# Performance work log

Measured on AMD Instinct MI355X. Metric: run time of the kernel, lower is better.

## Reference

```python
import jax, jax.numpy as jnp
from jax import lax
import numpy as np

VTH = 0.2
DECAY = 0.25            # LIF membrane decay used by pcdmd slayers.LIFSpike (STBP-style)
DT = 0.001              # norse default integration step
TAU_SYN_INV = 200.0     # norse LSNNParameters defaults
TAU_MEM_INV = 100.0
TAU_ADAPT_INV = 1.0 / 700.0
BETA = 0.0              # module sets beta=0 (no threshold adaptation jumps)
ALPHA = 100.0           # SuperSpike surrogate slope (norse 'super' method)

@jax.custom_vjp
def spike_rect(v):
    # Heaviside forward, rectangular surrogate backward (STBP)
    return (v > 0).astype(v.dtype)

def _sr_fwd(v):
    return spike_rect(v), v

def _sr_bwd(v, g):
    return (g * (jnp.abs(v) < 0.5).astype(g.dtype),)

spike_rect.defvjp(_sr_fwd, _sr_bwd)

@jax.custom_vjp
def spike_super(v):
    # Heaviside forward, SuperSpike surrogate backward (norse 'super')
    return (v > 0).astype(v.dtype)

def _ss_fwd(v):
    return spike_super(v), v

def _ss_bwd(v, g):
    return (g / (ALPHA * jnp.abs(v) + 1.0) ** 2,)

spike_super.defvjp(_ss_fwd, _ss_bwd)

def lif_spike(x):
    # x: [..., T] -> spike train [..., T]
    # u_t = DECAY * u_{t-1} * (1 - o_{t-1}) + x_t ; o_t = H(u_t - VTH)
    xT = jnp.moveaxis(x, -1, 0)  # [T, ...]
    u0 = jnp.zeros(xT.shape[1:], x.dtype)
    def step(carry, xt):
        u, o = carry
        u = DECAY * u * (1.0 - o) + xt
        o = spike_rect(u - VTH)
        return (u, o), o
    _, out = lax.scan(step, (u0, u0), xT)
    return jnp.moveaxis(out, 0, -1)

def lsnn_recurrent(x, w_in, w_rec):
    # x: [T, B, H] input spikes; norse LSNNRecurrent lsnn_step with beta=0, v_th=VTH
    x_in = jnp.einsum('tbh,oh->tbo', x, w_in)  # input current, hoisted out of scan
    B, H = x.shape[1], w_in.shape[0]
    z0 = jnp.zeros((B, H), x.dtype)
    state0 = (z0, z0, z0, jnp.full((B, H), VTH, x.dtype))  # z, v, i, b (b starts at v_th)
    def step(state, xt):
        z, v, i, b = state
        i_jump = i + xt + z @ w_rec.T
        v_dec = v + DT * TAU_MEM_INV * (-v + i_jump)          # v_leak = 0
        i_dec = i_jump - DT * TAU_SYN_INV * i_jump
        b_dec = b + DT * TAU_ADAPT_INV * (VTH - b)
        z_new = spike_super(v_dec - b_dec)
        v_new = (1.0 - z_new) * v_dec                          # v_reset = 0
        b_new = b_dec + z_new * TAU_ADAPT_INV * BETA
        return (z_new, v_new, i_dec, b_new), z_new
    _, out = lax.scan(step, state0, x_in)
    return out  # [T, B, H]

def setup_inputs() -> dict:
    key = jax.random.key(0)
    ks = jax.random.split(key, 7)
    B, T = 64, 8192
    EEG_C, AUD_C, H, OUT = 64, 1, 10, 2
    x = jax.random.normal(ks[0], (B, 1, EEG_C + 2 * AUD_C, T), jnp.float32)
    s_in = 1.0 / float(np.sqrt(EEG_C))
    s_h = 1.0 / float(np.sqrt(H))
    return {
        'x': x,
        'w_front': jax.random.uniform(ks[1], (H, EEG_C), jnp.float32, -s_in, s_in),
        'b_front': jax.random.uniform(ks[2], (H,), jnp.float32, -s_in, s_in),
        'w_in': jax.random.uniform(ks[3], (H, H), jnp.float32, -s_h, s_h),
        'w_rec': jax.random.uniform(ks[4], (H, H), jnp.float32, -s_h, s_h),
        'w_cls': jax.random.uniform(ks[5], (OUT, H), jnp.float32, -s_h, s_h),
        'b_cls': jax.random.uniform(ks[6], (OUT,), jnp.float32, -s_h, s_h),
    }

def reference(x, w_front, b_front, w_in, w_rec, w_cls, b_cls):
    AUD_C = 1
    window_length = x.shape[-1]
    eeg = x[:, 0, AUD_C:-AUD_C, :]                              # [B, 64, T]
    eeg = jnp.einsum('bct,hc->bht', eeg, w_front) + b_front[None, :, None]
    eeg = lif_spike(eeg)                                        # spike_tanh in snn mode
    eeg = jnp.transpose(eeg, (2, 0, 1))                         # [T, B, H]
    z = lsnn_recurrent(eeg, w_in, w_rec)                        # [T, B, H]
    out = jnp.transpose(z, (1, 2, 0))                           # [B, H, T]
    out = jnp.einsum('bht,oh->bot', out, w_cls) + b_cls[None, :, None]
    out = lif_spike(out)                                        # spike_sigmoid in snn mode
    return jnp.sum(out, axis=2) / window_length                 # [B, 2]
```

## Files before the change

### kernel.cpp

```cpp
#include <hip/hip_runtime.h>
#include <cstdint>
#include <cstddef>

#define T_LEN 8192
#define BATCH 64
#define HID   10
#define CH    66
#define EEG   64
#define SM_STRIDE 8384

__global__ void k_front(const float* __restrict__ x, const float* __restrict__ wf_g,
                        const float* __restrict__ bf_g, float* __restrict__ y) {
    __shared__ float wf[EEG][HID];
    __shared__ float bf[HID];
    int tid = threadIdx.x;
    for (int i = tid; i < EEG * HID; i += 256) {
        int h = i / EEG, c = i % EEG;
        wf[c][h] = wf_g[i];
    }
    if (tid < HID) bf[tid] = bf_g[tid];
    __syncthreads();

    int b = blockIdx.y;
    int t4 = (blockIdx.x * 256 + tid) * 4;
    const float* xb = x + ((size_t)b * CH + 1) * T_LEN + t4;
    float acc[4][HID];
#pragma unroll
    for (int j = 0; j < 4; ++j)
#pragma unroll
        for (int h = 0; h < HID; ++h) acc[j][h] = bf[h];
#pragma unroll 4
    for (int c = 0; c < EEG; ++c) {
        float4 xv = *(const float4*)(xb + (size_t)c * T_LEN);
#pragma unroll
        for (int h = 0; h < HID; ++h) {
            float w = wf[c][h];
            acc[0][h] = fmaf(xv.x, w, acc[0][h]);
            acc[1][h] = fmaf(xv.y, w, acc[1][h]);
            acc[2][h] = fmaf(xv.z, w, acc[2][h]);
            acc[3][h] = fmaf(xv.w, w, acc[3][h]);
        }
    }
    float* yo = y + (size_t)b * HID * T_LEN + t4;
#pragma unroll
    for (int h = 0; h < HID; ++h)
        *(float4*)(yo + (size_t)h * T_LEN) =
            make_float4(acc[0][h], acc[1][h], acc[2][h], acc[3][h]);
}

__global__ __launch_bounds__(64) void k_flif(const float* __restrict__ y,
                                             unsigned short* __restrict__ smask) {
    int c    = blockIdx.x >> 4;
    int bq   = blockIdx.x & 15;
    int lane = threadIdx.x;
    int g = lane >> 4, h = lane & 15;
    int b = bq * 4 + g;
    int hh = h < HID ? h : HID - 1;

    if (c == 0) {
        for (int i = lane; i < 4 * 96; i += 64) {
            int j = i / 96, w = i % 96;
            ((unsigned*)(smask + (size_t)(bq * 4 + j) * SM_STRIDE))[w] = 0u;
        }
    }

    int t0 = c * 256;
    int ts = t0 - 32; if (ts < 0) ts = 0;
    int nf = (t0 + 256 - ts) >> 2;
    const float4* yb = (const float4*)(y + ((size_t)b * HID + hh) * T_LEN + ts);

    float4 A = yb[0], B = yb[1];
    float u = 0.f, o = 0.f;
    unsigned short* smb = smask + (size_t)b * SM_STRIDE + 192;
    for (int f = 0; f < nf; ++f) {
        int nx = f + 2; if (nx > nf - 1) nx = nf - 1;
        float4 C = yb[nx];
        float vv[4] = {A.x, A.y, A.z, A.w};
        int tb = ts + f * 4;
#pragma unroll
        for (int k = 0; k < 4; ++k) {
            u = (o > 0.5f) ? vv[k] : fmaf(0.25f, u, vv[k]);
            bool sp = (u > 0.2f);
            o = sp ? 1.0f : 0.0f;
            unsigned long long bal = __ballot(sp);
            int t = tb + k;
            if (t >= t0 && h == 0)
                smb[t] = (unsigned short)((bal >> (g * 16)) & 0x3FFull);
        }
        A = B; B = C;
    }
}

__global__ __launch_bounds__(64) void k_lsnn(
    const unsigned short* __restrict__ smask,
    const float* __restrict__ w_in, const float* __restrict__ w_rec,
    const float* __restrict__ w_cls, const float* __restrict__ b_cls,
    float* __restrict__ out) {
    __shared__ float T[1536];
    int lane = threadIdx.x;
    for (int i = lane; i < 1536; i += 64) {
        int hi = i / 768;
        int rem = i - hi * 768;
        int m = rem / 24, role = rem - m * 24;
        float s = 0.f;
        if (role < 22) {
            const float* wrow = (role < 10) ? (w_in + role * HID)
                              : (role < 12) ? (w_cls + (role - 10) * HID)
                                            : (w_rec + (role - 12) * HID);
#pragma unroll
            for (int j = 0; j < 5; ++j)
                if (m & (1u << j)) s += wrow[hi * 5 + j];
        }
        T[i] = s;
    }
    __syncthreads();

    int q = lane >> 4;
    int r = lane & 15;
    int rr = r < 12 ? r : 11;
    int rrec = 12 + (r < HID ? r : 9);
    int shq = q * 16;
    int id = blockIdx.x * 4 + q;
    int b = id >> 7, chunk = id & 127;

    float bcl = (r == 10 || r == 11) ? b_cls[r - HID] : 0.f;

    const unsigned short* sm = smask + (size_t)b * SM_STRIDE + (size_t)chunk * 64;

    auto xlook = [&](const uint4& mv, float* X) {
        unsigned hw[8] = { mv.x & 0x3FFu, (mv.x >> 16) & 0x3FFu,
                           mv.y & 0x3FFu, (mv.y >> 16) & 0x3FFu,
                           mv.z & 0x3FFu, (mv.z >> 16) & 0x3FFu,
                           mv.w & 0x3FFu, (mv.w >> 16) & 0x3FFu };
#pragma unroll
        for (int u = 0; u < 8; ++u)
            X[u] = T[(hw[u] & 31u) * 24 + rr] + T[768 + (hw[u] >> 5) * 24 + rr];
    };

    uint4 mB = *(const uint4*)(sm + 8);
    uint4 mC = *(const uint4*)(sm + 16);
    uint4 mD = *(const uint4*)(sm + 24);
    float Xc[8], Xn[8], Pc[8], Pn[8];
    { uint4 m0 = *(const uint4*)(sm); xlook(m0, Xc); }
#pragma unroll
    for (int u = 0; u < 8; ++u) { Pc[u] = 0.f; Pn[u] = 0.f; }

    float v = 0.f, cur = 0.f;
    unsigned zmask = 0;
    float uc = 0.f, oc = 0.f, accs = 0.f;

    for (int gr = 0; gr < 32; ++gr) {
        int nb = gr + 4; if (nb > 31) nb = 31;
        uint4 mE = *(const uint4*)(sm + (size_t)nb * 8);
        xlook(mB, Xn);
        unsigned zs[8];
#pragma unroll
        for (int u = 0; u < 8; ++u) {
            float rec = T[(zmask & 31u) * 24 + rrec] + T[768 + (zmask >> 5) * 24 + rrec];
            float ij = (cur + Xc[u]) + rec;
            float vd = v + 0.1f * (ij - v);
            cur = ij - 0.2f * ij;
            bool zb = vd > 0.2f;
            unsigned long long bal = __ballot(zb);
            v = zb ? 0.f : vd;
            zmask = (unsigned)(bal >> shq) & 0x3FFu;
            zs[u] = zmask;
        }
        if (gr >= 21) {
#pragma unroll
            for (int u = 0; u < 8; ++u)
                Pn[u] = T[(zs[u] & 31u) * 24 + rr] + T[768 + (zs[u] >> 5) * 24 + rr];
        }
        if (gr >= 22) {
            bool in = (gr >= 25);
#pragma unroll
            for (int u = 0; u < 8; ++u) {
                float ci = Pc[u] + bcl;
                uc = (oc > 0.5f) ? ci : fmaf(0.25f, uc, ci);
                oc = (uc > 0.2f) ? 1.f : 0.f;
                if (in) accs += oc;
            }
        }
#pragma unroll
        for (int u = 0; u < 8; ++u) { Xc[u] = Xn[u]; Pc[u] = Pn[u]; }
        mB = mC; mC = mD; mD = mE;
    }
#pragma unroll
    for (int u = 0; u < 8; ++u) {
        float ci = Pc[u] + bcl;
        uc = (oc > 0.5f) ? ci : fmaf(0.25f, uc, ci);
        oc = (uc > 0.2f) ? 1.f : 0.f;
        accs += oc;
    }
    if (r == 10 || r == 11)
        atomicAdd(&out[b * 2 + (r - 10)], accs * (1.0f / 8192.0f));
}

extern "C" void kernel_launch(void* const* d_in, const int* in_sizes, int n_in,
                              void* d_out, int out_size, void* d_ws, size_t ws_size,
                              hipStream_t stream) {
    const float* x       = (const float*)d_in[0];
    const float* w_front = (const float*)d_in[1];
    const float* b_front = (const float*)d_in[2];
    const float* w_in    = (const float*)d_in[3];
    const float* w_rec   = (const float*)d_in[4];
    const float* w_cls   = (const float*)d_in[5];
    const float* b_cls   = (const float*)d_in[6];
    float* out = (float*)d_out;

    float* y = (float*)d_ws;
    unsigned short* smask =
        (unsigned short*)((char*)d_ws + (size_t)BATCH * HID * T_LEN * sizeof(float));

    hipMemsetAsync(out, 0, (size_t)out_size * sizeof(float), stream);
    k_front<<<dim3(T_LEN / 1024, BATCH), 256, 0, stream>>>(x, w_front, b_front, y);
    k_flif<<<dim3(512), 64, 0, stream>>>(y, smask);
    k_lsnn<<<dim3(2048), 64, 0, stream>>>(smask, w_in, w_rec, w_cls, b_cls, out);
}
```

Before: 313.3 us.

## Use full 1024-entry mask lookup tables and finer LIF chunks

k_lsnn now builds a 1024x22 table in LDS that maps each 10-bit spike mask directly to its summed weights. This replaces two table reads plus an add with a single read on the serial recurrent critical path. Blocks grow to 512 threads so the table build is shared across more work. k_flif splits time into 64-step chunks with a 32-step warmup over 2048 blocks for more parallelism, with a deeper prefetch. The cost is about 96KB of LDS per block, which limits occupancy, plus a larger share of redundant warmup work in k_flif.

```diff
diff --git a/kernel.cpp b/kernel.cpp
--- a/kernel.cpp
+++ b/kernel.cpp
@@ -50,8 +50,9 @@
 
 __global__ __launch_bounds__(64) void k_flif(const float* __restrict__ y,
                                              unsigned short* __restrict__ smask) {
-    int c    = blockIdx.x >> 4;
-    int bq   = blockIdx.x & 15;
+    int id = blockIdx.x;
+    int c  = (id & 7) * 16 + ((id >> 3) & 15);
+    int bq = id >> 7;
     int lane = threadIdx.x;
     int g = lane >> 4, h = lane & 15;
     int b = bq * 4 + g;
@@ -64,17 +65,17 @@
         }
     }
 
-    int t0 = c * 256;
+    int t0 = c * 64;
     int ts = t0 - 32; if (ts < 0) ts = 0;
-    int nf = (t0 + 256 - ts) >> 2;
+    int nf = (t0 + 64 - ts) >> 2;
     const float4* yb = (const float4*)(y + ((size_t)b * HID + hh) * T_LEN + ts);
 
-    float4 A = yb[0], B = yb[1];
+    float4 A = yb[0], B = yb[1], C = yb[2];
     float u = 0.f, o = 0.f;
     unsigned short* smb = smask + (size_t)b * SM_STRIDE + 192;
     for (int f = 0; f < nf; ++f) {
-        int nx = f + 2; if (nx > nf - 1) nx = nf - 1;
-        float4 C = yb[nx];
+        int nx = f + 3; if (nx > nf - 1) nx = nf - 1;
+        float4 D = yb[nx];
         float vv[4] = {A.x, A.y, A.z, A.w};
         int tb = ts + f * 4;
 #pragma unroll
@@ -87,18 +88,20 @@
             if (t >= t0 && h == 0)
                 smb[t] = (unsigned short)((bal >> (g * 16)) & 0x3FFull);
         }
-        A = B; B = C;
-    }
-}
-
-__global__ __launch_bounds__(64) void k_lsnn(
+        A = B; B = C; C = D;
+    }
+}
+
+__global__ __launch_bounds__(512) void k_lsnn(
     const unsigned short* __restrict__ smask,
     const float* __restrict__ w_in, const float* __restrict__ w_rec,
     const float* __restrict__ w_cls, const float* __restrict__ b_cls,
     float* __restrict__ out) {
-    __shared__ float T[1536];
-    int lane = threadIdx.x;
-    for (int i = lane; i < 1536; i += 64) {
+    extern __shared__ float LDSBUF[];
+    float* T = LDSBUF;
+    float* D = LDSBUF + 1536;
+    int tid = threadIdx.x;
+    for (int i = tid; i < 1536; i += 512) {
         int hi = i / 768;
         int rem = i - hi * 768;
         int m = rem / 24, role = rem - m * 24;
@@ -114,13 +117,19 @@
         T[i] = s;
     }
     __syncthreads();
-
+    for (int i = tid; i < 1024 * 22; i += 512) {
+        int z = i / 22, role = i - z * 22;
+        D[i] = T[(z & 31) * 24 + role] + T[768 + (z >> 5) * 24 + role];
+    }
+    __syncthreads();
+
+    int lane = tid & 63;
     int q = lane >> 4;
     int r = lane & 15;
     int rr = r < 12 ? r : 11;
     int rrec = 12 + (r < HID ? r : 9);
     int shq = q * 16;
-    int id = blockIdx.x * 4 + q;
+    int id = blockIdx.x * 32 + (tid >> 4);
     int b = id >> 7, chunk = id & 127;
 
     float bcl = (r == 10 || r == 11) ? b_cls[r - HID] : 0.f;
@@ -134,7 +143,7 @@
                            mv.w & 0x3FFu, (mv.w >> 16) & 0x3FFu };
 #pragma unroll
         for (int u = 0; u < 8; ++u)
-            X[u] = T[(hw[u] & 31u) * 24 + rr] + T[768 + (hw[u] >> 5) * 24 + rr];
+            X[u] = D[hw[u] * 22 + rr];
     };
 
     uint4 mB = *(const uint4*)(sm + 8);
@@ -156,7 +165,7 @@
         unsigned zs[8];
 #pragma unroll
         for (int u = 0; u < 8; ++u) {
-            float rec = T[(zmask & 31u) * 24 + rrec] + T[768 + (zmask >> 5) * 24 + rrec];
+            float rec = D[zmask * 22 + rrec];
             float ij = (cur + Xc[u]) + rec;
             float vd = v + 0.1f * (ij - v);
             cur = ij - 0.2f * ij;
@@ -169,7 +178,7 @@
         if (gr >= 21) {
 #pragma unroll
             for (int u = 0; u < 8; ++u)
-                Pn[u] = T[(zs[u] & 31u) * 24 + rr] + T[768 + (zs[u] >> 5) * 24 + rr];
+                Pn[u] = D[zs[u] * 22 + rr];
         }
         if (gr >= 22) {
             bool in = (gr >= 25);
@@ -214,6 +223,7 @@
 
     hipMemsetAsync(out, 0, (size_t)out_size * sizeof(float), stream);
     k_front<<<dim3(T_LEN / 1024, BATCH), 256, 0, stream>>>(x, w_front, b_front, y);
-    k_flif<<<dim3(512), 64, 0, stream>>>(y, smask);
-    k_lsnn<<<dim3(2048), 64, 0, stream>>>(smask, w_in, w_rec, w_cls, b_cls, out);
-}
+    k_flif<<<dim3(2048), 64, 0, stream>>>(y, smask);
+    k_lsnn<<<dim3(256), 512, (1536 + 1024 * 22) * sizeof(float), stream>>>(
+        smask, w_in, w_rec, w_cls, b_cls, out);
+}
```

New measurement: 279.5 us. -10.8%, faster.
